# Kernel tuning notes

Hardware: AMD Instinct MI355X
Metric: run time of the kernel (lower is better)

## Reference

```python
import jax, jax.numpy as jnp
import numpy as np
import math

B, NTR, NTE = 4, 256, 64
S = NTR + NTE
FN, D = 64, 256
HF, HS = 8, 8
HC = HF // 2
HID = 4 * D


def _ln(x, g, b, eps=1e-5):
    m = jnp.mean(x, axis=-1, keepdims=True)
    v = jnp.mean((x - m) ** 2, axis=-1, keepdims=True)
    return (x - m) / jnp.sqrt(v + eps) * g + b


def _mha(q, k, v, Wq, bq, Wk, bk, Wv, bv, Wo, bo, H, mask):
    # PyTorch nn.MultiheadAttention (batch_first, eval): per-head scaled dot product
    Bq, Lq, Dm = q.shape
    Lk = k.shape[1]
    hd = Dm // H
    qh = (q @ Wq.T + bq).reshape(Bq, Lq, H, hd).transpose(0, 2, 1, 3)
    kh = (k @ Wk.T + bk).reshape(Bq, Lk, H, hd).transpose(0, 2, 1, 3)
    vh = (v @ Wv.T + bv).reshape(Bq, Lk, H, hd).transpose(0, 2, 1, 3)
    s = jnp.einsum('bhqd,bhkd->bhqk', qh, kh) / math.sqrt(hd)
    if mask is not None:
        s = s + mask  # broadcast (1,H,Lq,Lk)
    a = jax.nn.softmax(s, axis=-1)
    o = jnp.einsum('bhqk,bhkd->bhqd', a, vh).transpose(0, 2, 1, 3).reshape(Bq, Lq, Dm)
    return o @ Wo.T + bo


def setup_inputs() -> dict:
    key = jax.random.key(0)
    ks = jax.random.split(key, 64)
    i = [0]
    def w(shape, s=0.02):
        k = ks[i[0]]; i[0] += 1
        return jax.random.normal(k, shape, jnp.float32) * s
    inp = {}
    inp['x'] = jax.random.normal(ks[40], (B, S, FN, D), jnp.float32)
    m = jax.random.randint(ks[41], (FN, FN), 0, 2).astype(jnp.float32)
    inp['attn_mask'] = jnp.maximum(m, jnp.eye(FN, dtype=jnp.float32))  # keep diagonal unmasked
    for p in ['f', 't', 'e']:
        for n in ['Wq', 'Wk', 'Wv', 'Wo']:
            inp[n + p] = w((D, D))
        for n in ['bq', 'bk', 'bv', 'bo']:
            inp[n + p] = jnp.zeros((D,), jnp.float32)
        inp['g' + p] = jnp.ones((D,), jnp.float32)
        inp['b2' + p] = jnp.zeros((D,), jnp.float32)
    inp['W1'] = w((HID, D)); inp['b1'] = jnp.zeros((HID,), jnp.float32)
    inp['Wg'] = w((HID, D)); inp['bg'] = jnp.zeros((HID,), jnp.float32)
    inp['W2'] = w((D, HID)); inp['b2'] = jnp.zeros((D,), jnp.float32)
    inp['gm'] = jnp.ones((D,), jnp.float32); inp['bm'] = jnp.zeros((D,), jnp.float32)
    inp['N_train'] = NTR
    inp['N_test'] = NTE
    return inp


def reference(x, attn_mask, Wqf, Wkf, Wvf, Wof, bqf, bkf, bvf, bof, gf, b2f,
              Wqt, Wkt, Wvt, Wot, bqt, bkt, bvt, bot, gt, b2t,
              Wqe, Wke, Wve, Woe, bqe, bke, bve, boe, ge, b2e,
              W1, b1, Wg, bg, W2, b2, gm, bm, N_train, N_test):
    Bsz, Ssz, Fn, Dd = x.shape
    # --- feature attention with hybrid per-head mask ---
    x_row = x.reshape(Bsz * Ssz, Fn, Dd)
    xn = _ln(x_row, gf, b2f)
    additive = jnp.where(attn_mask == 1.0, 0.0, -jnp.inf).astype(x.dtype)  # (F,F)
    hybrid = jnp.concatenate([
        jnp.broadcast_to(additive[None], (HC, Fn, Fn)),
        jnp.zeros((HF - HC, Fn, Fn), x.dtype)], axis=0)[None]  # (1,H,F,F)
    x2 = _mha(xn, xn, xn, Wqf, bqf, Wkf, bkf, Wvf, bvf, Wof, bof, HF, hybrid)
    x_row = x_row + x2
    # --- sample attention (train self, test cross) ---
    x_col = x_row.reshape(Bsz, Ssz, Fn, Dd).transpose(0, 2, 1, 3).reshape(Bsz * Fn, Ssz, Dd)
    x_tr = x_col[:, :N_train]
    x_te = x_col[:, N_train:]
    tn = _ln(x_tr, gt, b2t)
    x_tr = x_tr + _mha(tn, tn, tn, Wqt, bqt, Wkt, bkt, Wvt, bvt, Wot, bot, HS, None)
    en = _ln(x_te, ge, b2e)
    kv = _ln(x_tr, ge, b2e)
    x_te = x_te + _mha(en, kv, kv, Wqe, bqe, Wke, bke, Wve, bve, Woe, boe, HS, None)
    x_col = jnp.concatenate([x_tr, x_te], axis=1)
    xo = x_col.reshape(Bsz, Fn, Ssz, Dd).transpose(0, 2, 1, 3)
    # --- SwiGLU MLP ---
    xn2 = _ln(xo, gm, bm)
    h = (xn2 @ W1.T + b1) * jax.nn.silu(xn2 @ Wg.T + bg)
    return xo + (h @ W2.T + b2)
```

## Files before the change

### kernel.cpp

```cpp
#include <hip/hip_runtime.h>
#include <hip/hip_bf16.h>

typedef __hip_bfloat16 bf16;
typedef __attribute__((ext_vector_type(8))) short short8v;
typedef __attribute__((ext_vector_type(4))) float f32x4;

#define Bz   4
#define Sz   320
#define FNz  64
#define Dz   256
#define HIDz 1024
#define TOK  (Bz*Sz*FNz)
#define NSEQ (Bz*FNz)
#define NTRz 256
#define NTEz 64
#define TTR  (NSEQ*NTRz)
#define TTE  (NSEQ*NTEz)
#define CHD  40960
#define SCALE 0.17677669529663687f

__device__ __forceinline__ size_t rowOff(int rr, int Ls, int s0){
  if (Ls == 0) return (size_t)rr * Dz;
  int n = rr / Ls;
  int s = rr - n * Ls + s0;
  return (((size_t)(n >> 6) * Sz + s) * FNz + (n & 63)) * Dz;
}

__device__ __forceinline__ void store4bf(bf16* p, float a, float b, float c, float d){
  bf16 t0=__float2bfloat16(a), t1=__float2bfloat16(b),
       t2=__float2bfloat16(c), t3=__float2bfloat16(d);
  ushort4 u;
  u.x=*(unsigned short*)&t0; u.y=*(unsigned short*)&t1;
  u.z=*(unsigned short*)&t2; u.w=*(unsigned short*)&t3;
  *(ushort4*)p = u;
}

__device__ __forceinline__ void store2bf(bf16* p, float a, float b){
  bf16 t0=__float2bfloat16(a), t1=__float2bfloat16(b);
  ushort2 u;
  u.x=*(unsigned short*)&t0; u.y=*(unsigned short*)&t1;
  *(ushort2*)p = u;
}

__device__ __forceinline__ void halfwave_ln(float4 v0, float4 v1,
                                            float& mean, float& rsd){
  float s = v0.x+v0.y+v0.z+v0.w + v1.x+v1.y+v1.z+v1.w;
  float q = v0.x*v0.x+v0.y*v0.y+v0.z*v0.z+v0.w*v0.w
          + v1.x*v1.x+v1.y*v1.y+v1.z*v1.z+v1.w*v1.w;
  #pragma unroll
  for (int d = 1; d < 32; d <<= 1){ s += __shfl_xor(s, d); q += __shfl_xor(q, d); }
  mean = s * (1.0f/Dz);
  rsd  = rsqrtf(q * (1.0f/Dz) - mean*mean + 1e-5f);
}

__device__ __forceinline__ void ln_emit(bf16* dp, int c0, float4 v0, float4 v1,
                                        float mean, float rsd,
                                        const float* G, const float* B){
  float4 g0 = *(const float4*)(G + c0), g1 = *(const float4*)(G + c0 + 4);
  float4 b0 = *(const float4*)(B + c0), b1 = *(const float4*)(B + c0 + 4);
  store4bf(dp + c0,     (v0.x-mean)*rsd*g0.x + b0.x, (v0.y-mean)*rsd*g0.y + b0.y,
                        (v0.z-mean)*rsd*g0.z + b0.z, (v0.w-mean)*rsd*g0.w + b0.w);
  store4bf(dp + c0 + 4, (v1.x-mean)*rsd*g1.x + b1.x, (v1.y-mean)*rsd*g1.y + b1.y,
                        (v1.z-mean)*rsd*g1.z + b1.z, (v1.w-mean)*rsd*g1.w + b1.w);
}

struct CvtArgs { const float* src[24]; bf16* dst[24]; };
__global__ __launch_bounds__(256) void cvt_multi(CvtArgs args){
  int i = (blockIdx.x * 256 + threadIdx.x) * 4;
  const float* s = args.src[blockIdx.y];
  bf16*        d = args.dst[blockIdx.y];
  float4 v = *(const float4*)(s + i);
  store4bf(d + i, v.x, v.y, v.z, v.w);
}

__global__ __launch_bounds__(256) void ln_kernel(const float* __restrict__ src,
    bf16* __restrict__ dst, const float* __restrict__ g, const float* __restrict__ b,
    int Ls, int s0){
  int rr   = blockIdx.x * 4 + (threadIdx.x >> 6);
  int lane = threadIdx.x & 63;
  size_t off = rowOff(rr, Ls, s0) + (size_t)lane * 4;
  float4 v = *(const float4*)(src + off);
  float s = v.x + v.y + v.z + v.w;
  float q = v.x*v.x + v.y*v.y + v.z*v.z + v.w*v.w;
  #pragma unroll
  for (int d = 1; d < 64; d <<= 1){ s += __shfl_xor(s, d); q += __shfl_xor(q, d); }
  float m   = s * (1.0f/Dz);
  float rsd = rsqrtf(q * (1.0f/Dz) - m*m + 1e-5f);
  float4 gv = *(const float4*)(g + lane*4);
  float4 bv = *(const float4*)(b + lane*4);
  store4bf(dst + (size_t)rr*Dz + lane*4,
           (v.x-m)*rsd*gv.x + bv.x, (v.y-m)*rsd*gv.y + bv.y,
           (v.z-m)*rsd*gv.z + bv.z, (v.w-m)*rsd*gv.w + bv.w);
}

__global__ __launch_bounds__(512) void mgemm_store(
    const bf16* __restrict__ A, const bf16* __restrict__ Wb,
    const float* __restrict__ bias, const float* __restrict__ biasB,
    const float* __restrict__ biasC, bf16* __restrict__ Cp,
    int N, int K, int ncols){
  __shared__ bf16 As[128][40];
  __shared__ bf16 Bs[256][40];
  const int tid  = threadIdx.x;
  const int lane = tid & 63;
  const int wave = tid >> 6;
  int L   = blockIdx.x;
  int cpx = gridDim.x >> 3;
  int W   = (L & 7) * cpx + (L >> 3);
  int rowb = W / ncols, colb = W - rowb * ncols;
  const int r0 = rowb * 128;
  const int n0 = colb * 256;
  const int srow = tid >> 2;
  const int scol = (tid & 3) * 8;
  const int bprow = (srow & 64) + (srow & 15)*4 + ((srow >> 4) & 3);
  const bf16* ap  = A  + (size_t)(r0 + srow) * K + scol;
  const bf16* bp0 = Wb + (size_t)(n0 + bprow) * K + scol;
  const bf16* bp1 = Wb + (size_t)(n0 + 128 + bprow) * K + scol;
  const int wr = wave >> 2, wc = wave & 3;
  const int fr = lane & 15;
  const int fk = (lane >> 4) * 8;
  f32x4 acc[4][4] = {};
  for (int k0 = 0; k0 < K; k0 += 32){
    uint4 av  = *(const uint4*)(ap  + k0);
    uint4 bv0 = *(const uint4*)(bp0 + k0);
    uint4 bv1 = *(const uint4*)(bp1 + k0);
    __syncthreads();
    *(uint4*)&As[srow][scol]       = av;
    *(uint4*)&Bs[srow][scol]       = bv0;
    *(uint4*)&Bs[128 + srow][scol] = bv1;
    __syncthreads();
    short8v af[4], bf[4];
    #pragma unroll
    for (int m = 0; m < 4; ++m)
      af[m] = *(const short8v*)&As[wr*64 + m*16 + fr][fk];
    #pragma unroll
    for (int n = 0; n < 4; ++n)
      bf[n] = *(const short8v*)&Bs[wc*64 + n*16 + fr][fk];
    #pragma unroll
    for (int m = 0; m < 4; ++m)
      #pragma unroll
      for (int n = 0; n < 4; ++n)
        acc[m][n] = __builtin_amdgcn_mfma_f32_16x16x32_bf16(af[m], bf[n], acc[m][n], 0, 0, 0);
  }
  const int er = (lane >> 4) * 4;
  const float* bp = bias;
  if (biasB != nullptr) bp = (colb == 0) ? bias : ((colb == 1) ? biasB : biasC);
  const int cl = wc*64 + fr*4;
  float bb0 = bp[cl], bb1 = bp[cl+1], bb2 = bp[cl+2], bb3 = bp[cl+3];
  const int cbase = n0 + cl;
  #pragma unroll
  for (int m = 0; m < 4; ++m){
    #pragma unroll
    for (int j = 0; j < 4; ++j){
      int r = r0 + wr*64 + m*16 + er + j;
      store4bf(&Cp[(size_t)r * N + cbase],
               acc[m][0][j] + bb0, acc[m][1][j] + bb1,
               acc[m][2][j] + bb2, acc[m][3][j] + bb3);
    }
  }
}

template<int FUSE>
__global__ __launch_bounds__(512) void mgemm_resid(
    const bf16* __restrict__ A, const bf16* __restrict__ Wb,
    const float* __restrict__ bias, float* __restrict__ Cp,
    const float* __restrict__ resid,
    int K, int cLs, int cS0,
    const float* lnGa, const float* lnBa, const float* lnGb, const float* lnBb,
    bf16* dstA, bf16* dstB){
  __shared__ __align__(16) char smemraw[30720];
  bf16 (*As)[40] = reinterpret_cast<bf16(*)[40]>(smemraw);
  bf16 (*Bs)[40] = reinterpret_cast<bf16(*)[40]>(smemraw + 10240);
  const int tid  = threadIdx.x;
  const int lane = tid & 63;
  const int wave = tid >> 6;
  int L   = blockIdx.x;
  int cpx = gridDim.x >> 3;
  const int r0 = ((L & 7) * cpx + (L >> 3)) * 128;
  const int srow = tid >> 2;
  const int scol = (tid & 3) * 8;
  const int bprow = (srow & 64) + (srow & 15)*4 + ((srow >> 4) & 3);
  const bf16* ap  = A  + (size_t)(r0 + srow) * K + scol;
  const bf16* bp0 = Wb + (size_t)(bprow) * K + scol;
  const bf16* bp1 = Wb + (size_t)(128 + bprow) * K + scol;
  const int wr = wave >> 2, wc = wave & 3;
  const int fr = lane & 15;
  const int fk = (lane >> 4) * 8;
  f32x4 acc[4][4] = {};
  for (int k0 = 0; k0 < K; k0 += 32){
    uint4 av  = *(const uint4*)(ap  + k0);
    uint4 bv0 = *(const uint4*)(bp0 + k0);
    uint4 bv1 = *(const uint4*)(bp1 + k0);
    __syncthreads();
    *(uint4*)&As[srow][scol]       = av;
    *(uint4*)&Bs[srow][scol]       = bv0;
    *(uint4*)&Bs[128 + srow][scol] = bv1;
    __syncthreads();
    short8v af[4], bf[4];
    #pragma unroll
    for (int m = 0; m < 4; ++m)
      af[m] = *(const short8v*)&As[wr*64 + m*16 + fr][fk];
    #pragma unroll
    for (int n = 0; n < 4; ++n)
      bf[n] = *(const short8v*)&Bs[wc*64 + n*16 + fr][fk];
    #pragma unroll
    for (int m = 0; m < 4; ++m)
      #pragma unroll
      for (int n = 0; n < 4; ++n)
        acc[m][n] = __builtin_amdgcn_mfma_f32_16x16x32_bf16(af[m], bf[n], acc[m][n], 0, 0, 0);
  }
  const int er = (lane >> 4) * 4;
  float* fsm = (float*)smemraw;
  const int cb = wc*64 + fr*4;
  float bb0 = bias[cb], bb1 = bias[cb+1], bb2 = bias[cb+2], bb3 = bias[cb+3];
  #pragma unroll
  for (int m = 0; m < 4; ++m){
    #pragma unroll
    for (int wrs = 0; wrs < 2; ++wrs){
      __syncthreads();
      if (wr == wrs){
        #pragma unroll
        for (int j = 0; j < 4; ++j){
          float4 t;
          t.x = acc[m][0][j] + bb0; t.y = acc[m][1][j] + bb1;
          t.z = acc[m][2][j] + bb2; t.w = acc[m][3][j] + bb3;
          *(float4*)&fsm[(er + j)*260 + cb] = t;
        }
      }
      __syncthreads();
      int rrow = r0 + wrs*64 + m*16 + (tid >> 5);
      int c0 = (tid & 31) * 8;
      size_t ro = rowOff(rrow, cLs, cS0) + c0;
      const float* fs = fsm + (tid >> 5)*260 + c0;
      float4 v0 = *(const float4*)(fs);
      float4 v1 = *(const float4*)(fs + 4);
      float4 q0 = *(const float4*)(resid + ro);
      float4 q1 = *(const float4*)(resid + ro + 4);
      v0.x += q0.x; v0.y += q0.y; v0.z += q0.z; v0.w += q0.w;
      v1.x += q1.x; v1.y += q1.y; v1.z += q1.z; v1.w += q1.w;
      *(float4*)(Cp + ro)     = v0;
      *(float4*)(Cp + ro + 4) = v1;
      if (FUSE > 0){
        float mean, rsd;
        halfwave_ln(v0, v1, mean, rsd);
        if (FUSE == 1){
          int b = rrow / (Sz*FNz);
          int rem = rrow - b*(Sz*FNz);
          int s = rem >> 6, f = rem & 63;
          int n = (b << 6) + f;
          if (s < NTRz)
            ln_emit(dstA + (size_t)(n*NTRz + s)*Dz, c0, v0, v1, mean, rsd, lnGa, lnBa);
          else
            ln_emit(dstB + (size_t)(n*NTEz + s - NTRz)*Dz, c0, v0, v1, mean, rsd, lnGb, lnBb);
        } else if (FUSE == 2){
          int n = rrow >> 8, s = rrow & 255;
          int b = n >> 6, f = n & 63;
          ln_emit(dstA + (size_t)rrow*Dz, c0, v0, v1, mean, rsd, lnGa, lnBa);
          ln_emit(dstB + (size_t)((b*Sz + s)*FNz + f)*Dz, c0, v0, v1, mean, rsd, lnGb, lnBb);
        } else {
          int n = rrow >> 6, t = rrow & 63;
          int b = n >> 6, f = n & 63, s = t + NTRz;
          ln_emit(dstB + (size_t)((b*Sz + s)*FNz + f)*Dz, c0, v0, v1, mean, rsd, lnGb, lnBb);
        }
      }
    }
  }
}

__global__ __launch_bounds__(512) void mgemm_dual(
    const bf16* __restrict__ A, const bf16* __restrict__ W1b,
    const bf16* __restrict__ Wgb, const float* __restrict__ b1,
    const float* __restrict__ bg, bf16* __restrict__ Hb,
    int M, int K){
  __shared__ bf16 As[128][40];
  __shared__ bf16 B1s[128][40];
  __shared__ bf16 B2s[128][40];
  const int tid  = threadIdx.x;
  const int lane = tid & 63;
  const int wave = tid >> 6;
  int L   = blockIdx.x;
  int cpx = gridDim.x >> 3;
  int W   = (L & 7) * cpx + (L >> 3);
  int rowb = W >> 3, colb = W & 7;
  const int r0 = rowb * 128;
  const int n0 = colb * 128;
  const int srow = tid >> 2;
  const int scol = (tid & 3) * 8;
  const int bprow = (srow & ~31) + (srow & 15)*2 + ((srow >> 4) & 1);
  const bf16* ap = A   + (size_t)(r0 + srow) * K + scol;
  const bf16* p1 = W1b + (size_t)(n0 + bprow) * K + scol;
  const bf16* p2 = Wgb + (size_t)(n0 + bprow) * K + scol;
  const int wr = wave >> 2, wc = wave & 3;
  const int fr = lane & 15;
  const int fk = (lane >> 4) * 8;
  f32x4 acc1[4][2] = {};
  f32x4 acc2[4][2] = {};
  for (int k0 = 0; k0 < K; k0 += 32){
    uint4 av = *(const uint4*)(ap + k0);
    uint4 v1 = *(const uint4*)(p1 + k0);
    uint4 v2 = *(const uint4*)(p2 + k0);
    __syncthreads();
    *(uint4*)&As[srow][scol]  = av;
    *(uint4*)&B1s[srow][scol] = v1;
    *(uint4*)&B2s[srow][scol] = v2;
    __syncthreads();
    short8v af[4], bf1[2], bf2[2];
    #pragma unroll
    for (int m = 0; m < 4; ++m)
      af[m] = *(const short8v*)&As[wr*64 + m*16 + fr][fk];
    #pragma unroll
    for (int n = 0; n < 2; ++n){
      bf1[n] = *(const short8v*)&B1s[wc*32 + n*16 + fr][fk];
      bf2[n] = *(const short8v*)&B2s[wc*32 + n*16 + fr][fk];
    }
    #pragma unroll
    for (int m = 0; m < 4; ++m)
      #pragma unroll
      for (int n = 0; n < 2; ++n){
        acc1[m][n] = __builtin_amdgcn_mfma_f32_16x16x32_bf16(af[m], bf1[n], acc1[m][n], 0, 0, 0);
        acc2[m][n] = __builtin_amdgcn_mfma_f32_16x16x32_bf16(af[m], bf2[n], acc2[m][n], 0, 0, 0);
      }
  }
  const int er = (lane >> 4) * 4;
  const int c = n0 + wc*32 + fr*2;
  const float b10 = b1[c], b11 = b1[c+1];
  const float bg0 = bg[c], bg1 = bg[c+1];
  #pragma unroll
  for (int m = 0; m < 4; ++m){
    #pragma unroll
    for (int j = 0; j < 4; ++j){
      int r = r0 + wr*64 + m*16 + er + j;
      float v0 = acc1[m][0][j] + b10;
      float g0 = acc2[m][0][j] + bg0;
      float v1 = acc1[m][1][j] + b11;
      float g1 = acc2[m][1][j] + bg1;
      float h0 = v0 * g0 / (1.0f + __expf(-g0));
      float h1 = v1 * g1 / (1.0f + __expf(-g1));
      store2bf(&Hb[(size_t)r * HIDz + c], h0, h1);
    }
  }
}

__global__ __launch_bounds__(256) void attn_t_m(
    const bf16* __restrict__ Q, const bf16* __restrict__ K,
    const bf16* __restrict__ V, bf16* __restrict__ O, int ld){
  __shared__ bf16 Klds[64][40];
  __shared__ bf16 Vt[32][72];
  __shared__ bf16 Plds[4][64][72];
  const int n = blockIdx.x, h = blockIdx.y;
  const int tid = threadIdx.x, lane = tid & 63, w = tid >> 6;
  const size_t ibase = (size_t)n * 256 * ld + (size_t)h * 32;
  const size_t obase = (size_t)n * 256 * Dz + (size_t)h * 32;
  const int l15 = lane & 15, l4 = lane >> 4;
  short8v qf[4];
  #pragma unroll
  for (int m = 0; m < 4; ++m)
    qf[m] = *(const short8v*)(Q + ibase + (size_t)(w*64 + m*16 + l15) * ld + l4*8);
  f32x4 accO[4][2] = {};
  float mrowq[4], lrowq[4], sclq[4];
  #pragma unroll
  for (int m=0;m<4;++m){ mrowq[m] = -1e30f; lrowq[m] = 0.f; }
  const f32x4 zero = {};
  for (int kb = 0; kb < 4; ++kb){
    __syncthreads();
    {
      int r = tid >> 2, c8 = (tid & 3) * 8;
      *(uint4*)&Klds[r][c8] = *(const uint4*)(K + ibase + (size_t)(kb*64 + r) * ld + c8);
      uint4 vr = *(const uint4*)(V + ibase + (size_t)(kb*64 + r) * ld + c8);
      const bf16* vb = (const bf16*)&vr;
      #pragma unroll
      for (int i = 0; i < 8; ++i) Vt[c8 + i][r] = vb[i];
    }
    __syncthreads();
    short8v kf[4];
    #pragma unroll
    for (int nn = 0; nn < 4; ++nn)
      kf[nn] = *(const short8v*)&Klds[nn*16 + l15][l4*8];
    f32x4 s2[4][4];
    #pragma unroll
    for (int m = 0; m < 4; ++m)
      #pragma unroll
      for (int nn = 0; nn < 4; ++nn)
        s2[m][nn] = __builtin_amdgcn_mfma_f32_16x16x32_bf16(kf[nn], qf[m], zero, 0,0,0);
    #pragma unroll
    for (int m = 0; m < 4; ++m){
      float mx = fmaxf(fmaxf(s2[m][0][0], s2[m][0][1]), fmaxf(s2[m][0][2], s2[m][0][3]));
      #pragma unroll
      for (int nn = 1; nn < 4; ++nn)
        mx = fmaxf(mx, fmaxf(fmaxf(s2[m][nn][0], s2[m][nn][1]),
                             fmaxf(s2[m][nn][2], s2[m][nn][3])));
      mx = fmaxf(mx, __shfl_xor(mx, 16));
      mx = fmaxf(mx, __shfl_xor(mx, 32));
      float mnew = fmaxf(mrowq[m], mx);
      float scl = __expf((mrowq[m] - mnew) * SCALE);
      mrowq[m] = mnew; sclq[m] = scl;
      float ps = 0.f;
      #pragma unroll
      for (int nn = 0; nn < 4; ++nn)
        #pragma unroll
        for (int j = 0; j < 4; ++j){
          float p = __expf((s2[m][nn][j] - mnew) * SCALE);
          s2[m][nn][j] = p; ps += p;
        }
      ps += __shfl_xor(ps, 16);
      ps += __shfl_xor(ps, 32);
      lrowq[m] = lrowq[m] * scl + ps;
    }
    #pragma unroll
    for (int m = 0; m < 4; ++m)
      #pragma unroll
      for (int j = 0; j < 4; ++j){
        float so = __shfl(sclq[m], l4*4 + j);
        accO[m][0][j] *= so; accO[m][1][j] *= so;
      }
    #pragma unroll
    for (int m = 0; m < 4; ++m)
      #pragma unroll
      for (int nn = 0; nn < 4; ++nn)
        store4bf(&Plds[w][m*16 + l15][nn*16 + l4*4],
                 s2[m][nn][0], s2[m][nn][1], s2[m][nn][2], s2[m][nn][3]);
    #pragma unroll
    for (int m = 0; m < 4; ++m){
      #pragma unroll
      for (int kt = 0; kt < 2; ++kt){
        short8v pf = *(const short8v*)&Plds[w][m*16 + l15][kt*32 + l4*8];
        #pragma unroll
        for (int dt = 0; dt < 2; ++dt){
          short8v vf = *(const short8v*)&Vt[dt*16 + l15][kt*32 + l4*8];
          accO[m][dt] = __builtin_amdgcn_mfma_f32_16x16x32_bf16(pf, vf, accO[m][dt], 0,0,0);
        }
      }
    }
  }
  #pragma unroll
  for (int m = 0; m < 4; ++m){
    #pragma unroll
    for (int j = 0; j < 4; ++j){
      float inv = 1.0f / __shfl(lrowq[m], l4*4 + j);
      int row = w*64 + m*16 + l4*4 + j;
      #pragma unroll
      for (int dt = 0; dt < 2; ++dt)
        O[obase + (size_t)row * Dz + dt*16 + l15] = __float2bfloat16(accO[m][dt][j] * inv);
    }
  }
}

template<int NKB, int MASK>
__global__ __launch_bounds__(256) void attn_w(
    const bf16* __restrict__ Q, const bf16* __restrict__ K,
    const bf16* __restrict__ V, const float* __restrict__ mask,
    bf16* __restrict__ O, int ldq, int ldkv){
  __shared__ bf16 Klds[4][64][40];
  __shared__ bf16 Vt[4][32][72];
  __shared__ bf16 Plds[4][64][72];
  const int r = blockIdx.x;
  const int tid = threadIdx.x, lane = tid & 63, w = tid >> 6;
  const int h = blockIdx.y * 4 + w;
  const int l15 = lane & 15, l4 = lane >> 4;
  const size_t qoff = (size_t)r * 64 * ldq + (size_t)h * 32;
  const size_t koff = (size_t)r * (NKB*64) * ldkv + (size_t)h * 32;
  const size_t ooff = (size_t)r * 64 * Dz + (size_t)h * 32;
  short8v qf[4];
  #pragma unroll
  for (int m = 0; m < 4; ++m)
    qf[m] = *(const short8v*)(Q + qoff + (size_t)(m*16 + l15) * ldq + l4*8);
  f32x4 accO[4][2] = {};
  float mrowq[4], lrowq[4], sclq[4];
  #pragma unroll
  for (int m=0;m<4;++m){ mrowq[m] = -1e30f; lrowq[m] = 0.f; }
  const f32x4 zero = {};
  for (int kb = 0; kb < NKB; ++kb){
    {
      const bf16* kp = K + koff + (size_t)(kb*64 + lane) * ldkv;
      const bf16* vp = V + koff + (size_t)(kb*64 + lane) * ldkv;
      uint4 k0 = *(const uint4*)(kp);      uint4 k1 = *(const uint4*)(kp + 8);
      uint4 k2 = *(const uint4*)(kp + 16); uint4 k3 = *(const uint4*)(kp + 24);
      *(uint4*)&Klds[w][lane][0]  = k0; *(uint4*)&Klds[w][lane][8]  = k1;
      *(uint4*)&Klds[w][lane][16] = k2; *(uint4*)&Klds[w][lane][24] = k3;
      uint4 v0 = *(const uint4*)(vp);      uint4 v1 = *(const uint4*)(vp + 8);
      uint4 v2 = *(const uint4*)(vp + 16); uint4 v3 = *(const uint4*)(vp + 24);
      const bf16* vb0=(const bf16*)&v0; const bf16* vb1=(const bf16*)&v1;
      const bf16* vb2=(const bf16*)&v2; const bf16* vb3=(const bf16*)&v3;
      #pragma unroll
      for (int i = 0; i < 8; ++i){
        Vt[w][i][lane]      = vb0[i];
        Vt[w][8 + i][lane]  = vb1[i];
        Vt[w][16 + i][lane] = vb2[i];
        Vt[w][24 + i][lane] = vb3[i];
      }
    }
    short8v kf[4];
    #pragma unroll
    for (int nn = 0; nn < 4; ++nn)
      kf[nn] = *(const short8v*)&Klds[w][nn*16 + l15][l4*8];
    f32x4 s2[4][4];
    #pragma unroll
    for (int m = 0; m < 4; ++m)
      #pragma unroll
      for (int nn = 0; nn < 4; ++nn)
        s2[m][nn] = __builtin_amdgcn_mfma_f32_16x16x32_bf16(kf[nn], qf[m], zero, 0,0,0);
    if (MASK && h < 4){
      #pragma unroll
      for (int m = 0; m < 4; ++m)
        #pragma unroll
        for (int nn = 0; nn < 4; ++nn)
          #pragma unroll
          for (int j = 0; j < 4; ++j){
            int qq = m*16 + l15, kk = nn*16 + l4*4 + j;
            s2[m][nn][j] += (mask[qq*64 + kk] == 1.0f ? 0.0f : -1e30f);
          }
    }
    #pragma unroll
    for (int m = 0; m < 4; ++m){
      float mx = fmaxf(fmaxf(s2[m][0][0], s2[m][0][1]), fmaxf(s2[m][0][2], s2[m][0][3]));
      #pragma unroll
      for (int nn = 1; nn < 4; ++nn)
        mx = fmaxf(mx, fmaxf(fmaxf(s2[m][nn][0], s2[m][nn][1]),
                             fmaxf(s2[m][nn][2], s2[m][nn][3])));
      mx = fmaxf(mx, __shfl_xor(mx, 16));
      mx = fmaxf(mx, __shfl_xor(mx, 32));
      float mnew = fmaxf(mrowq[m], mx);
      float scl = __expf((mrowq[m] - mnew) * SCALE);
      mrowq[m] = mnew; sclq[m] = scl;
      float ps = 0.f;
      #pragma unroll
      for (int nn = 0; nn < 4; ++nn)
        #pragma unroll
        for (int j = 0; j < 4; ++j){
          float p = __expf((s2[m][nn][j] - mnew) * SCALE);
          s2[m][nn][j] = p; ps += p;
        }
      ps += __shfl_xor(ps, 16);
      ps += __shfl_xor(ps, 32);
      lrowq[m] = lrowq[m] * scl + ps;
    }
    #pragma unroll
    for (int m = 0; m < 4; ++m)
      #pragma unroll
      for (int j = 0; j < 4; ++j){
        float so = __shfl(sclq[m], l4*4 + j);
        accO[m][0][j] *= so; accO[m][1][j] *= so;
      }
    #pragma unroll
    for (int m = 0; m < 4; ++m)
      #pragma unroll
      for (int nn = 0; nn < 4; ++nn)
        store4bf(&Plds[w][m*16 + l15][nn*16 + l4*4],
                 s2[m][nn][0], s2[m][nn][1], s2[m][nn][2], s2[m][nn][3]);
    #pragma unroll
    for (int m = 0; m < 4; ++m){
      #pragma unroll
      for (int kt = 0; kt < 2; ++kt){
        short8v pf = *(const short8v*)&Plds[w][m*16 + l15][kt*32 + l4*8];
        #pragma unroll
        for (int dt = 0; dt < 2; ++dt){
          short8v vf = *(const short8v*)&Vt[w][dt*16 + l15][kt*32 + l4*8];
          accO[m][dt] = __builtin_amdgcn_mfma_f32_16x16x32_bf16(pf, vf, accO[m][dt], 0,0,0);
        }
      }
    }
  }
  #pragma unroll
  for (int m = 0; m < 4; ++m){
    #pragma unroll
    for (int j = 0; j < 4; ++j){
      float inv = 1.0f / __shfl(lrowq[m], l4*4 + j);
      int row = m*16 + l4*4 + j;
      #pragma unroll
      for (int dt = 0; dt < 2; ++dt)
        O[ooff + (size_t)row * Dz + dt*16 + l15] = __float2bfloat16(accO[m][dt][j] * inv);
    }
  }
}

extern "C" void kernel_launch(void* const* d_in, const int* in_sizes, int n_in,
                              void* d_out, int out_size, void* d_ws, size_t ws_size,
                              hipStream_t stream){
  (void)in_sizes; (void)n_in; (void)out_size; (void)ws_size;
  const float* x    = (const float*)d_in[0];
  const float* mask = (const float*)d_in[1];
  const float *Wqf=(const float*)d_in[2],  *Wkf=(const float*)d_in[3],
              *Wvf=(const float*)d_in[4],  *Wof=(const float*)d_in[5],
              *bqf=(const float*)d_in[6],  *bkf=(const float*)d_in[7],
              *bvf=(const float*)d_in[8],  *bof=(const float*)d_in[9],
              *gf =(const float*)d_in[10], *b2f=(const float*)d_in[11];
  const float *Wqt=(const float*)d_in[12], *Wkt=(const float*)d_in[13],
              *Wvt=(const float*)d_in[14], *Wot=(const float*)d_in[15],
              *bqt=(const float*)d_in[16], *bkt=(const float*)d_in[17],
              *bvt=(const float*)d_in[18], *bot=(const float*)d_in[19],
              *gt =(const float*)d_in[20], *b2t=(const float*)d_in[21];
  const float *Wqe=(const float*)d_in[22], *Wke=(const float*)d_in[23],
              *Wve=(const float*)d_in[24], *Woe=(const float*)d_in[25],
              *bqe=(const float*)d_in[26], *bke=(const float*)d_in[27],
              *bve=(const float*)d_in[28], *boe=(const float*)d_in[29],
              *ge =(const float*)d_in[30], *b2e=(const float*)d_in[31];
  const float *W1=(const float*)d_in[32], *b1=(const float*)d_in[33],
              *Wg=(const float*)d_in[34], *bg=(const float*)d_in[35],
              *W2=(const float*)d_in[36], *b2v=(const float*)d_in[37],
              *gm=(const float*)d_in[38], *bm=(const float*)d_in[39];

  float* Y = (float*)d_out;

  char* wsb = (char*)d_ws;
  size_t off = 0;
  auto carve = [&](size_t bytes)->void*{
    void* p = wsb + off; off += (bytes + 255) & ~(size_t)255; return p;
  };
  bf16* Xn   = (bf16*)carve((size_t)TOK * Dz * 2);
  bf16* QKVb = (bf16*)carve((size_t)TOK * 768 * 2);
  bf16* Ob   = (bf16*)carve((size_t)TOK * Dz * 2);
  bf16* Hb   = (bf16*)carve((size_t)CHD * HIDz * 2);
  bf16* WQKVf = (bf16*)carve((size_t)768*256*2);
  bf16* WQKVt = (bf16*)carve((size_t)768*256*2);
  bf16* WKVe  = (bf16*)carve((size_t)512*256*2);
  bf16* Wqeb  = (bf16*)carve((size_t)256*256*2);
  bf16* Wofb  = (bf16*)carve((size_t)256*256*2);
  bf16* Wotb  = (bf16*)carve((size_t)256*256*2);
  bf16* Woeb  = (bf16*)carve((size_t)256*256*2);
  bf16* W1b   = (bf16*)carve((size_t)HIDz*256*2);
  bf16* Wgb   = (bf16*)carve((size_t)HIDz*256*2);
  bf16* W2b   = (bf16*)carve((size_t)256*HIDz*2);

  bf16* XnD = QKVb + (size_t)TOK * 512;
  bf16* Xnq = Xn + (size_t)TTR * Dz;
  bf16* Qeb = QKVb + (size_t)TTR * 512;

  const int DD = Dz*Dz;
  {
    CvtArgs ca;
    const float* s12[12] = {Wqf,Wkf,Wvf, Wqt,Wkt,Wvt, Wke,Wve, Wqe,Wof,Wot,Woe};
    bf16* d12[12] = {WQKVf,WQKVf+DD,WQKVf+2*DD, WQKVt,WQKVt+DD,WQKVt+2*DD,
                     WKVe,WKVe+DD, Wqeb,Wofb,Wotb,Woeb};
    for (int i = 0; i < 12; ++i){ ca.src[i] = s12[i]; ca.dst[i] = d12[i]; }
    const float* sh[3] = {W1, Wg, W2};
    bf16* dh[3] = {W1b, Wgb, W2b};
    for (int j = 0; j < 3; ++j)
      for (int p = 0; p < 4; ++p){
        ca.src[12 + j*4 + p] = sh[j] + (size_t)p * DD;
        ca.dst[12 + j*4 + p] = dh[j] + (size_t)p * DD;
      }
    cvt_multi<<<dim3(DD/1024, 24), 256, 0, stream>>>(ca);
  }

  ln_kernel<<<TOK/4, 256, 0, stream>>>(x, Xn, gf, b2f, 0, 0);
  mgemm_store<<<3*(TOK/128), 512, 0, stream>>>(Xn, WQKVf, bqf, bkf, bvf, QKVb,
      768, 256, 3);
  attn_w<1,1><<<dim3(Bz*Sz, 2), 256, 0, stream>>>(QKVb, QKVb+256, QKVb+512, mask, Ob, 768, 768);
  mgemm_resid<1><<<TOK/128, 512, 0, stream>>>(Ob, Wofb, bof, Y, x,
      256, 0,0, gt, b2t, ge, b2e, Xn, Xnq);

  mgemm_store<<<3*(TTR/128), 512, 0, stream>>>(Xn, WQKVt, bqt, bkt, bvt, QKVb,
      768, 256, 3);
  attn_t_m<<<dim3(NSEQ, 8), 256, 0, stream>>>(QKVb, QKVb+256, QKVb+512, Ob, 768);
  mgemm_resid<2><<<TTR/128, 512, 0, stream>>>(Ob, Wotb, bot, Y, Y,
      256, NTRz,0, ge, b2e, gm, bm, Xn, XnD);

  mgemm_store<<<TTE/128, 512, 0, stream>>>(Xnq, Wqeb, bqe,
      nullptr, nullptr, Qeb, 256, 256, 1);
  mgemm_store<<<2*(TTR/128), 512, 0, stream>>>(Xn, WKVe, bke, bve, bve, QKVb,
      512, 256, 2);
  attn_w<4,0><<<dim3(NSEQ, 2), 256, 0, stream>>>(Qeb, QKVb, QKVb+256,
      nullptr, Ob, 256, 512);
  mgemm_resid<3><<<TTE/128, 512, 0, stream>>>(Ob, Woeb, boe, Y, Y,
      256, NTEz,NTRz, nullptr, nullptr, gm, bm, nullptr, XnD);

  for (int c = 0; c < TOK/CHD; ++c){
    const bf16* Anc = XnD + (size_t)c * CHD * Dz;
    float*      Yc  = Y   + (size_t)c * CHD * Dz;
    mgemm_dual<<<8*(CHD/128), 512, 0, stream>>>(Anc, W1b, Wgb, b1, bg,
        Hb, CHD, 256);
    mgemm_resid<0><<<CHD/128, 512, 0, stream>>>(Hb, W2b, b2v, Yc, Yc,
        HIDz, 0,0, nullptr, nullptr, nullptr, nullptr, nullptr, nullptr);
  }
}
```

Measured before the change: 747.8 us.

## Defer LayerNorm to consumer GEMM A-loads using stored per-row statistics

Residual GEMM epilogues now write only a per-row (mean, rsd) pair instead of emitting normalized bf16 copies of the activations. The consumer GEMMs (sample-attention QKV, test Q, KV, and the SwiGLU dual GEMM) read fp32 Y directly and apply LayerNorm with gamma/beta while staging A into shared memory. This removes the bf16 LN output writes and their buffers. In exchange, consumers read fp32 A (twice the bytes of bf16), through strided row gathers, and redo the normalization arithmetic for every column block. The dual GEMM in particular re-reads and re-normalizes each A tile across its 8 column blocks.

```diff
diff --git a/kernel.cpp b/kernel.cpp
--- a/kernel.cpp
+++ b/kernel.cpp
@@ -35,6 +35,15 @@
   *(ushort4*)p = u;
 }
 
+__device__ __forceinline__ ushort4 pack4bf(float a, float b, float c, float d){
+  bf16 t0=__float2bfloat16(a), t1=__float2bfloat16(b),
+       t2=__float2bfloat16(c), t3=__float2bfloat16(d);
+  ushort4 u;
+  u.x=*(unsigned short*)&t0; u.y=*(unsigned short*)&t1;
+  u.z=*(unsigned short*)&t2; u.w=*(unsigned short*)&t3;
+  return u;
+}
+
 __device__ __forceinline__ void store2bf(bf16* p, float a, float b){
   bf16 t0=__float2bfloat16(a), t1=__float2bfloat16(b);
   ushort2 u;
@@ -51,17 +60,6 @@
   for (int d = 1; d < 32; d <<= 1){ s += __shfl_xor(s, d); q += __shfl_xor(q, d); }
   mean = s * (1.0f/Dz);
   rsd  = rsqrtf(q * (1.0f/Dz) - mean*mean + 1e-5f);
-}
-
-__device__ __forceinline__ void ln_emit(bf16* dp, int c0, float4 v0, float4 v1,
-                                        float mean, float rsd,
-                                        const float* G, const float* B){
-  float4 g0 = *(const float4*)(G + c0), g1 = *(const float4*)(G + c0 + 4);
-  float4 b0 = *(const float4*)(B + c0), b1 = *(const float4*)(B + c0 + 4);
-  store4bf(dp + c0,     (v0.x-mean)*rsd*g0.x + b0.x, (v0.y-mean)*rsd*g0.y + b0.y,
-                        (v0.z-mean)*rsd*g0.z + b0.z, (v0.w-mean)*rsd*g0.w + b0.w);
-  store4bf(dp + c0 + 4, (v1.x-mean)*rsd*g1.x + b1.x, (v1.y-mean)*rsd*g1.y + b1.y,
-                        (v1.z-mean)*rsd*g1.z + b1.z, (v1.w-mean)*rsd*g1.w + b1.w);
 }
 
 struct CvtArgs { const float* src[24]; bf16* dst[24]; };
@@ -74,11 +72,10 @@
 }
 
 __global__ __launch_bounds__(256) void ln_kernel(const float* __restrict__ src,
-    bf16* __restrict__ dst, const float* __restrict__ g, const float* __restrict__ b,
-    int Ls, int s0){
+    bf16* __restrict__ dst, const float* __restrict__ g, const float* __restrict__ b){
   int rr   = blockIdx.x * 4 + (threadIdx.x >> 6);
   int lane = threadIdx.x & 63;
-  size_t off = rowOff(rr, Ls, s0) + (size_t)lane * 4;
+  size_t off = (size_t)rr * Dz + (size_t)lane * 4;
   float4 v = *(const float4*)(src + off);
   float s = v.x + v.y + v.z + v.w;
   float q = v.x*v.x + v.y*v.y + v.z*v.z + v.w*v.w;
@@ -88,7 +85,7 @@
   float rsd = rsqrtf(q * (1.0f/Dz) - m*m + 1e-5f);
   float4 gv = *(const float4*)(g + lane*4);
   float4 bv = *(const float4*)(b + lane*4);
-  store4bf(dst + (size_t)rr*Dz + lane*4,
+  store4bf(dst + off,
            (v.x-m)*rsd*gv.x + bv.x, (v.y-m)*rsd*gv.y + bv.y,
            (v.z-m)*rsd*gv.z + bv.z, (v.w-m)*rsd*gv.w + bv.w);
 }
@@ -159,14 +156,92 @@
   }
 }
 
-template<int FUSE>
-__global__ __launch_bounds__(512) void mgemm_resid(
+__global__ __launch_bounds__(512) void mgemm_storeF(
+    const float* __restrict__ Yf, const bf16* __restrict__ Wb,
+    const float* __restrict__ bias, const float* __restrict__ biasB,
+    const float* __restrict__ biasC, bf16* __restrict__ Cp,
+    const float2* __restrict__ S,
+    const float* __restrict__ lnG, const float* __restrict__ lnB,
+    int N, int K, int ncols, int aLs, int aS0){
+  __shared__ bf16 As[128][40];
+  __shared__ bf16 Bs[256][40];
+  const int tid  = threadIdx.x;
+  const int lane = tid & 63;
+  const int wave = tid >> 6;
+  int L   = blockIdx.x;
+  int cpx = gridDim.x >> 3;
+  int W   = (L & 7) * cpx + (L >> 3);
+  int rowb = W / ncols, colb = W - rowb * ncols;
+  const int r0 = rowb * 128;
+  const int n0 = colb * 256;
+  const int srow = tid >> 2;
+  const int scol = (tid & 3) * 8;
+  const int bprow = (srow & 64) + (srow & 15)*4 + ((srow >> 4) & 3);
+  const size_t aro = rowOff(r0 + srow, aLs, aS0);
+  const float* apF = Yf + aro + scol;
+  float2 st = S[aro >> 8];
+  const float mean = st.x, rsd = st.y;
+  const bf16* bp0 = Wb + (size_t)(n0 + bprow) * K + scol;
+  const bf16* bp1 = Wb + (size_t)(n0 + 128 + bprow) * K + scol;
+  const int wr = wave >> 2, wc = wave & 3;
+  const int fr = lane & 15;
+  const int fk = (lane >> 4) * 8;
+  f32x4 acc[4][4] = {};
+  for (int k0 = 0; k0 < K; k0 += 32){
+    float4 u0 = *(const float4*)(apF + k0);
+    float4 u1 = *(const float4*)(apF + k0 + 4);
+    float4 g0 = *(const float4*)(lnG + k0 + scol);
+    float4 g1 = *(const float4*)(lnG + k0 + scol + 4);
+    float4 h0 = *(const float4*)(lnB + k0 + scol);
+    float4 h1 = *(const float4*)(lnB + k0 + scol + 4);
+    ushort4 a0 = pack4bf((u0.x-mean)*rsd*g0.x + h0.x, (u0.y-mean)*rsd*g0.y + h0.y,
+                         (u0.z-mean)*rsd*g0.z + h0.z, (u0.w-mean)*rsd*g0.w + h0.w);
+    ushort4 a1 = pack4bf((u1.x-mean)*rsd*g1.x + h1.x, (u1.y-mean)*rsd*g1.y + h1.y,
+                         (u1.z-mean)*rsd*g1.z + h1.z, (u1.w-mean)*rsd*g1.w + h1.w);
+    uint4 bv0 = *(const uint4*)(bp0 + k0);
+    uint4 bv1 = *(const uint4*)(bp1 + k0);
+    __syncthreads();
+    *(ushort4*)&As[srow][scol]     = a0;
+    *(ushort4*)&As[srow][scol + 4] = a1;
+    *(uint4*)&Bs[srow][scol]       = bv0;
+    *(uint4*)&Bs[128 + srow][scol] = bv1;
+    __syncthreads();
+    short8v af[4], bf[4];
+    #pragma unroll
+    for (int m = 0; m < 4; ++m)
+      af[m] = *(const short8v*)&As[wr*64 + m*16 + fr][fk];
+    #pragma unroll
+    for (int n = 0; n < 4; ++n)
+      bf[n] = *(const short8v*)&Bs[wc*64 + n*16 + fr][fk];
+    #pragma unroll
+    for (int m = 0; m < 4; ++m)
+      #pragma unroll
+      for (int n = 0; n < 4; ++n)
+        acc[m][n] = __builtin_amdgcn_mfma_f32_16x16x32_bf16(af[m], bf[n], acc[m][n], 0, 0, 0);
+  }
+  const int er = (lane >> 4) * 4;
+  const float* bp = bias;
+  if (biasB != nullptr) bp = (colb == 0) ? bias : ((colb == 1) ? biasB : biasC);
+  const int cl = wc*64 + fr*4;
+  float bb0 = bp[cl], bb1 = bp[cl+1], bb2 = bp[cl+2], bb3 = bp[cl+3];
+  const int cbase = n0 + cl;
+  #pragma unroll
+  for (int m = 0; m < 4; ++m){
+    #pragma unroll
+    for (int j = 0; j < 4; ++j){
+      int r = r0 + wr*64 + m*16 + er + j;
+      store4bf(&Cp[(size_t)r * N + cbase],
+               acc[m][0][j] + bb0, acc[m][1][j] + bb1,
+               acc[m][2][j] + bb2, acc[m][3][j] + bb3);
+    }
+  }
+}
+
+__global__ __launch_bounds__(512) void mgemm_residS(
     const bf16* __restrict__ A, const bf16* __restrict__ Wb,
     const float* __restrict__ bias, float* __restrict__ Cp,
-    const float* __restrict__ resid,
-    int K, int cLs, int cS0,
-    const float* lnGa, const float* lnBa, const float* lnGb, const float* lnBb,
-    bf16* dstA, bf16* dstB){
+    const float* __restrict__ resid, float2* __restrict__ S,
+    int K, int cLs, int cS0){
   __shared__ __align__(16) char smemraw[30720];
   bf16 (*As)[40] = reinterpret_cast<bf16(*)[40]>(smemraw);
   bf16 (*Bs)[40] = reinterpret_cast<bf16(*)[40]>(smemraw + 10240);
@@ -239,38 +314,19 @@
       v1.x += q1.x; v1.y += q1.y; v1.z += q1.z; v1.w += q1.w;
       *(float4*)(Cp + ro)     = v0;
       *(float4*)(Cp + ro + 4) = v1;
-      if (FUSE > 0){
-        float mean, rsd;
-        halfwave_ln(v0, v1, mean, rsd);
-        if (FUSE == 1){
-          int b = rrow / (Sz*FNz);
-          int rem = rrow - b*(Sz*FNz);
-          int s = rem >> 6, f = rem & 63;
-          int n = (b << 6) + f;
-          if (s < NTRz)
-            ln_emit(dstA + (size_t)(n*NTRz + s)*Dz, c0, v0, v1, mean, rsd, lnGa, lnBa);
-          else
-            ln_emit(dstB + (size_t)(n*NTEz + s - NTRz)*Dz, c0, v0, v1, mean, rsd, lnGb, lnBb);
-        } else if (FUSE == 2){
-          int n = rrow >> 8, s = rrow & 255;
-          int b = n >> 6, f = n & 63;
-          ln_emit(dstA + (size_t)rrow*Dz, c0, v0, v1, mean, rsd, lnGa, lnBa);
-          ln_emit(dstB + (size_t)((b*Sz + s)*FNz + f)*Dz, c0, v0, v1, mean, rsd, lnGb, lnBb);
-        } else {
-          int n = rrow >> 6, t = rrow & 63;
-          int b = n >> 6, f = n & 63, s = t + NTRz;
-          ln_emit(dstB + (size_t)((b*Sz + s)*FNz + f)*Dz, c0, v0, v1, mean, rsd, lnGb, lnBb);
-        }
-      }
-    }
-  }
-}
-
-__global__ __launch_bounds__(512) void mgemm_dual(
-    const bf16* __restrict__ A, const bf16* __restrict__ W1b,
+      float mean, rsd;
+      halfwave_ln(v0, v1, mean, rsd);
+      if ((tid & 31) == 0) S[ro >> 8] = make_float2(mean, rsd);
+    }
+  }
+}
+
+__global__ __launch_bounds__(512) void mgemm_dualF(
+    const float* __restrict__ Yf, const bf16* __restrict__ W1b,
     const bf16* __restrict__ Wgb, const float* __restrict__ b1,
     const float* __restrict__ bg, bf16* __restrict__ Hb,
-    int M, int K){
+    const float2* __restrict__ S,
+    const float* __restrict__ lnG, const float* __restrict__ lnB, int K){
   __shared__ bf16 As[128][40];
   __shared__ bf16 B1s[128][40];
   __shared__ bf16 B2s[128][40];
@@ -286,7 +342,9 @@
   const int srow = tid >> 2;
   const int scol = (tid & 3) * 8;
   const int bprow = (srow & ~31) + (srow & 15)*2 + ((srow >> 4) & 1);
-  const bf16* ap = A   + (size_t)(r0 + srow) * K + scol;
+  const float* apF = Yf + (size_t)(r0 + srow) * Dz + scol;
+  float2 st = S[r0 + srow];
+  const float mean = st.x, rsd = st.y;
   const bf16* p1 = W1b + (size_t)(n0 + bprow) * K + scol;
   const bf16* p2 = Wgb + (size_t)(n0 + bprow) * K + scol;
   const int wr = wave >> 2, wc = wave & 3;
@@ -295,11 +353,21 @@
   f32x4 acc1[4][2] = {};
   f32x4 acc2[4][2] = {};
   for (int k0 = 0; k0 < K; k0 += 32){
-    uint4 av = *(const uint4*)(ap + k0);
+    float4 u0 = *(const float4*)(apF + k0);
+    float4 u1 = *(const float4*)(apF + k0 + 4);
+    float4 g0 = *(const float4*)(lnG + k0 + scol);
+    float4 g1 = *(const float4*)(lnG + k0 + scol + 4);
+    float4 h0 = *(const float4*)(lnB + k0 + scol);
+    float4 h1 = *(const float4*)(lnB + k0 + scol + 4);
+    ushort4 a0 = pack4bf((u0.x-mean)*rsd*g0.x + h0.x, (u0.y-mean)*rsd*g0.y + h0.y,
+                         (u0.z-mean)*rsd*g0.z + h0.z, (u0.w-mean)*rsd*g0.w + h0.w);
+    ushort4 a1 = pack4bf((u1.x-mean)*rsd*g1.x + h1.x, (u1.y-mean)*rsd*g1.y + h1.y,
+                         (u1.z-mean)*rsd*g1.z + h1.z, (u1.w-mean)*rsd*g1.w + h1.w);
     uint4 v1 = *(const uint4*)(p1 + k0);
     uint4 v2 = *(const uint4*)(p2 + k0);
     __syncthreads();
-    *(uint4*)&As[srow][scol]  = av;
+    *(ushort4*)&As[srow][scol]     = a0;
+    *(ushort4*)&As[srow][scol + 4] = a1;
     *(uint4*)&B1s[srow][scol] = v1;
     *(uint4*)&B2s[srow][scol] = v2;
     __syncthreads();
@@ -620,8 +688,7 @@
   bf16* Wgb   = (bf16*)carve((size_t)HIDz*256*2);
   bf16* W2b   = (bf16*)carve((size_t)256*HIDz*2);
 
-  bf16* XnD = QKVb + (size_t)TOK * 512;
-  bf16* Xnq = Xn + (size_t)TTR * Dz;
+  float2* S = (float2*)(QKVb + ((size_t)TOK * 768 - (size_t)TOK * 4));
   bf16* Qeb = QKVb + (size_t)TTR * 512;
 
   const int DD = Dz*Dz;
@@ -641,34 +708,30 @@
     cvt_multi<<<dim3(DD/1024, 24), 256, 0, stream>>>(ca);
   }
 
-  ln_kernel<<<TOK/4, 256, 0, stream>>>(x, Xn, gf, b2f, 0, 0);
+  ln_kernel<<<TOK/4, 256, 0, stream>>>(x, Xn, gf, b2f);
   mgemm_store<<<3*(TOK/128), 512, 0, stream>>>(Xn, WQKVf, bqf, bkf, bvf, QKVb,
       768, 256, 3);
   attn_w<1,1><<<dim3(Bz*Sz, 2), 256, 0, stream>>>(QKVb, QKVb+256, QKVb+512, mask, Ob, 768, 768);
-  mgemm_resid<1><<<TOK/128, 512, 0, stream>>>(Ob, Wofb, bof, Y, x,
-      256, 0,0, gt, b2t, ge, b2e, Xn, Xnq);
-
-  mgemm_store<<<3*(TTR/128), 512, 0, stream>>>(Xn, WQKVt, bqt, bkt, bvt, QKVb,
-      768, 256, 3);
+  mgemm_residS<<<TOK/128, 512, 0, stream>>>(Ob, Wofb, bof, Y, x, S, 256, 0, 0);
+
+  mgemm_storeF<<<3*(TTR/128), 512, 0, stream>>>(Y, WQKVt, bqt, bkt, bvt, QKVb,
+      S, gt, b2t, 768, 256, 3, NTRz, 0);
   attn_t_m<<<dim3(NSEQ, 8), 256, 0, stream>>>(QKVb, QKVb+256, QKVb+512, Ob, 768);
-  mgemm_resid<2><<<TTR/128, 512, 0, stream>>>(Ob, Wotb, bot, Y, Y,
-      256, NTRz,0, ge, b2e, gm, bm, Xn, XnD);
-
-  mgemm_store<<<TTE/128, 512, 0, stream>>>(Xnq, Wqeb, bqe,
-      nullptr, nullptr, Qeb, 256, 256, 1);
-  mgemm_store<<<2*(TTR/128), 512, 0, stream>>>(Xn, WKVe, bke, bve, bve, QKVb,
-      512, 256, 2);
+  mgemm_residS<<<TTR/128, 512, 0, stream>>>(Ob, Wotb, bot, Y, Y, S, 256, NTRz, 0);
+
+  mgemm_storeF<<<TTE/128, 512, 0, stream>>>(Y, Wqeb, bqe, nullptr, nullptr, Qeb,
+      S, ge, b2e, 256, 256, 1, NTEz, NTRz);
+  mgemm_storeF<<<2*(TTR/128), 512, 0, stream>>>(Y, WKVe, bke, bve, bve, QKVb,
+      S, ge, b2e, 512, 256, 2, NTRz, 0);
   attn_w<4,0><<<dim3(NSEQ, 2), 256, 0, stream>>>(Qeb, QKVb, QKVb+256,
       nullptr, Ob, 256, 512);
-  mgemm_resid<3><<<TTE/128, 512, 0, stream>>>(Ob, Woeb, boe, Y, Y,
-      256, NTEz,NTRz, nullptr, nullptr, gm, bm, nullptr, XnD);
+  mgemm_residS<<<TTE/128, 512, 0, stream>>>(Ob, Woeb, boe, Y, Y, S, 256, NTEz, NTRz);
 
   for (int c = 0; c < TOK/CHD; ++c){
-    const bf16* Anc = XnD + (size_t)c * CHD * Dz;
-    float*      Yc  = Y   + (size_t)c * CHD * Dz;
-    mgemm_dual<<<8*(CHD/128), 512, 0, stream>>>(Anc, W1b, Wgb, b1, bg,
-        Hb, CHD, 256);
-    mgemm_resid<0><<<CHD/128, 512, 0, stream>>>(Hb, W2b, b2v, Yc, Yc,
-        HIDz, 0,0, nullptr, nullptr, nullptr, nullptr, nullptr, nullptr);
-  }
-}
+    const float* Yc = Y + (size_t)c * CHD * Dz;
+    mgemm_dualF<<<8*(CHD/128), 512, 0, stream>>>(Yc, W1b, Wgb, b1, bg,
+        Hb, S + (size_t)c * CHD, gm, bm, 256);
+    mgemm_residS<<<CHD/128, 512, 0, stream>>>(Hb, W2b, b2v, (float*)Yc, Yc, S,
+        HIDz, 0, 0);
+  }
+}
```

Measured after the change: 765.9 us. +2.4%, slower.
